# Kernel tuning notes

Hardware: AMD Instinct MI355X
Metric: run time of the kernel (lower is better)

The kernel has to match this reference:

```python
import jax, jax.numpy as jnp
import numpy as np

C_Z = 128
DIST_BINS = 39
MIN_BIN = 3.25
MAX_BIN = 50.75
IN_FEAT = DIST_BINS + 1 + 21 + 21  # 82


def setup_inputs() -> dict:
    key = jax.random.key(0)
    k1, k2, k3, k4, k5 = jax.random.split(key, 5)
    B, T, L = 2, 4, 384
    template_aatype = jax.random.randint(k1, (B, T, L), 0, 21)
    # scale coords so pair distances span the [3.25, 50.75] bin range
    template_ca_coords = 10.0 * jax.random.normal(k2, (B, T, L, 3), dtype=jnp.float32)
    template_ca_mask = jax.random.randint(k3, (B, T, L), 0, 2).astype(bool)
    residue_mask = jnp.ones((B, L), dtype=bool)
    weight = jax.random.normal(k4, (IN_FEAT, C_Z), dtype=jnp.float32) / np.sqrt(IN_FEAT)
    bias = 0.02 * jax.random.normal(k5, (C_Z,), dtype=jnp.float32)
    return dict(template_aatype=template_aatype,
                template_ca_coords=template_ca_coords,
                template_ca_mask=template_ca_mask,
                residue_mask=residue_mask,
                weight=weight, bias=bias)


def reference(template_aatype, template_ca_coords, template_ca_mask, residue_mask, weight, bias):
    # Pairwise CA distances (torch.cdist p=2): [B,T,L,L]
    diff = template_ca_coords[:, :, :, None, :] - template_ca_coords[:, :, None, :, :]
    d = jnp.sqrt(jnp.sum(diff * diff, axis=-1))
    boundaries = jnp.linspace(MIN_BIN, MAX_BIN, DIST_BINS - 1).astype(d.dtype)
    # torch.bucketize(right=False) == searchsorted side='left'
    d_bin = jnp.searchsorted(boundaries, d, side='left')
    aat = jnp.clip(template_aatype, 0, 20)
    # Linear(one_hot concat) == gather of the corresponding weight-row blocks.
    W_d = weight[:DIST_BINS]                       # [39, c_z]
    W_m = weight[DIST_BINS]                        # [c_z]
    W_i = weight[DIST_BINS + 1:DIST_BINS + 22]     # [21, c_z]
    W_j = weight[DIST_BINS + 22:]                  # [21, c_z]
    tmask_pair = (template_ca_mask[:, :, :, None] & template_ca_mask[:, :, None, :]).astype(jnp.float32)  # [B,T,L,L]
    emb = (W_d[d_bin]
           + tmask_pair[..., None] * W_m
           + W_i[aat][:, :, :, None, :]
           + W_j[aat][:, :, None, :, :]
           + bias)                                  # [B,T,L,L,c_z]
    emb = emb * tmask_pair[..., None]
    denom = jnp.maximum(tmask_pair.sum(axis=1), 1.0)[..., None]  # [B,L,L,1]
    z_tpl = emb.sum(axis=1) / denom                 # [B,L,L,c_z]
    res_pair = (residue_mask[:, :, None] & residue_mask[:, None, :]).astype(jnp.float32)[..., None]
    return z_tpl * res_pair
```

## Files before the change

### kernel.cpp

```cpp
#include <hip/hip_runtime.h>
#include <cstddef>

#define BB 2
#define TT 4
#define LL 384
#define CZ 128
#define NBINS 39
#define NBOUND 38

__global__ __launch_bounds__(512) void tpe_kernel(
    const int*   __restrict__ aatype,
    const float* __restrict__ coords,
    const int*   __restrict__ tmask,
    const int*   __restrict__ rmask,
    const float* __restrict__ weight,
    const float* __restrict__ bias,
    float*       __restrict__ out)
{
    __shared__ float Wd_sh[NBINS * CZ];
    __shared__ float Wj_sh[21 * CZ];
    __shared__ float ps_sh[16 * CZ];
    __shared__ int4  meta_sh[LL];

    const int bi  = blockIdx.x;
    const int b   = bi / LL;
    const int i   = bi - b * LL;
    const int tid = threadIdx.x;

    {
        const float4* wsrc = (const float4*)weight;
        float4* wd = (float4*)Wd_sh;
        for (int idx = tid; idx < NBINS * CZ / 4; idx += 512) wd[idx] = wsrc[idx];
        float4* wj = (float4*)Wj_sh;
        for (int idx = tid; idx < 21 * CZ / 4; idx += 512)
            wj[idx] = wsrc[(NBINS + 1 + 21) * CZ / 4 + idx];
    }

    for (int idx = tid; idx < 16 * CZ; idx += 512) {
        int code = idx >> 7, c = idx & (CZ - 1);
        float v = 0.0f;
        if (code) {
            float base = weight[NBINS * CZ + c] + bias[c];
            v = (float)__popc(code) * base;
            #pragma unroll
            for (int t = 0; t < TT; ++t) {
                if (code & (1 << t)) {
                    int aa = aatype[(b * TT + t) * LL + i];
                    aa = min(max(aa, 0), 20);
                    v += weight[(NBINS + 1 + aa) * CZ + c];
                }
            }
        }
        ps_sh[idx] = v;
    }

    {
        #pragma clang fp contract(off)
        const int ri = rmask[b * LL + i];
        for (int j = tid; j < LL; j += 512) {
            unsigned pk01 = 0, pk23 = 0;
            int code = 0;
            #pragma unroll
            for (int t = 0; t < TT; ++t) {
                const int base = (b * TT + t) * LL;
                unsigned pk = 0xFFFFu;
                if (tmask[base + i] != 0 && tmask[base + j] != 0) {
                    const float* ci = coords + (size_t)(base + i) * 3;
                    const float* cj = coords + (size_t)(base + j) * 3;
                    float dx = ci[0] - cj[0];
                    float dy = ci[1] - cj[1];
                    float dz = ci[2] - cj[2];
                    float s  = dx * dx + dy * dy;
                    s = s + dz * dz;
                    float d = sqrtf(s);
                    int bin = 0;
                    #pragma unroll
                    for (int k = 0; k < NBOUND; ++k) {
                        float bnd = (float)(3.25 + (double)k * (47.5 / 37.0));
                        bin += (d > bnd) ? 1 : 0;
                    }
                    int aa = aatype[base + j];
                    aa = min(max(aa, 0), 20);
                    pk = (unsigned)(bin | (aa << 6));
                    code |= (1 << t);
                }
                if (t < 2) pk01 |= pk << (16 * t);
                else       pk23 |= pk << (16 * (t - 2));
            }
            int cnt = __popc(code);
            float scale = (ri != 0 && rmask[b * LL + j] != 0)
                          ? 1.0f / fmaxf((float)cnt, 1.0f) : 0.0f;
            int4 m;
            m.x = (int)pk01; m.y = (int)pk23; m.z = code; m.w = __float_as_int(scale);
            meta_sh[j] = m;
        }
    }
    __syncthreads();

    const int cg = tid & 31;
    const int jj = tid >> 5;
    const float4* Wd4 = (const float4*)Wd_sh;
    const float4* Wj4 = (const float4*)Wj_sh;
    const float4* ps4 = (const float4*)ps_sh;
    float4* outv = (float4*)(out + (size_t)(b * LL + i) * LL * CZ);

    #pragma unroll 2
    for (int j = jj; j < LL; j += 16) {
        int4 m = meta_sh[j];
        const int code = m.z;
        const float scale = __int_as_float(m.w);
        float4 acc = ps4[code * (CZ / 4) + cg];
        const unsigned pk01 = (unsigned)m.x, pk23 = (unsigned)m.y;

        if (code & 1) {
            unsigned pk = pk01 & 0xFFFFu;
            float4 a = Wd4[(pk & 63u) * (CZ / 4) + cg];
            float4 c2 = Wj4[(pk >> 6) * (CZ / 4) + cg];
            acc.x += a.x + c2.x; acc.y += a.y + c2.y; acc.z += a.z + c2.z; acc.w += a.w + c2.w;
        }
        if (code & 2) {
            unsigned pk = pk01 >> 16;
            float4 a = Wd4[(pk & 63u) * (CZ / 4) + cg];
            float4 c2 = Wj4[(pk >> 6) * (CZ / 4) + cg];
            acc.x += a.x + c2.x; acc.y += a.y + c2.y; acc.z += a.z + c2.z; acc.w += a.w + c2.w;
        }
        if (code & 4) {
            unsigned pk = pk23 & 0xFFFFu;
            float4 a = Wd4[(pk & 63u) * (CZ / 4) + cg];
            float4 c2 = Wj4[(pk >> 6) * (CZ / 4) + cg];
            acc.x += a.x + c2.x; acc.y += a.y + c2.y; acc.z += a.z + c2.z; acc.w += a.w + c2.w;
        }
        if (code & 8) {
            unsigned pk = pk23 >> 16;
            float4 a = Wd4[(pk & 63u) * (CZ / 4) + cg];
            float4 c2 = Wj4[(pk >> 6) * (CZ / 4) + cg];
            acc.x += a.x + c2.x; acc.y += a.y + c2.y; acc.z += a.z + c2.z; acc.w += a.w + c2.w;
        }
        float4 o;
        o.x = acc.x * scale; o.y = acc.y * scale;
        o.z = acc.z * scale; o.w = acc.w * scale;
        outv[j * (CZ / 4) + cg] = o;
    }
}

extern "C" void kernel_launch(void* const* d_in, const int* in_sizes, int n_in,
                              void* d_out, int out_size, void* d_ws, size_t ws_size,
                              hipStream_t stream) {
    const int*   aatype = (const int*)d_in[0];
    const float* coords = (const float*)d_in[1];
    const int*   tmask  = (const int*)d_in[2];
    const int*   rmask  = (const int*)d_in[3];
    const float* weight = (const float*)d_in[4];
    const float* bias   = (const float*)d_in[5];
    float* out = (float*)d_out;

    dim3 grid(BB * LL);
    dim3 block(512);
    tpe_kernel<<<grid, block, 0, stream>>>(aatype, coords, tmask, rmask, weight, bias, out);
}
```

Measured before the change: 34.02 us.

## Prefetch weights into registers, compact per-pair template list, nontemporal output stores

Weight rows are loaded into registers at kernel start and written to shared memory only after the metadata pass, so the global-load latency overlaps with the ps table and distance-binning work. Valid templates are packed contiguously with a count, and the four branchy per-template blocks become a counted loop. Output is written with nontemporal stores because it is never reread, and the j loop unroll is raised to 4. In exchange the kernel holds more registers, and the accumulation order of template contributions changes slightly.

```diff
diff --git a/kernel.cpp b/kernel.cpp
--- a/kernel.cpp
+++ b/kernel.cpp
@@ -7,6 +7,8 @@
 #define CZ 128
 #define NBINS 39
 #define NBOUND 38
+
+typedef float f32x4 __attribute__((ext_vector_type(4)));
 
 __global__ __launch_bounds__(512) void tpe_kernel(
     const int*   __restrict__ aatype,
@@ -27,13 +29,13 @@
     const int i   = bi - b * LL;
     const int tid = threadIdx.x;
 
-    {
-        const float4* wsrc = (const float4*)weight;
-        float4* wd = (float4*)Wd_sh;
-        for (int idx = tid; idx < NBINS * CZ / 4; idx += 512) wd[idx] = wsrc[idx];
-        float4* wj = (float4*)Wj_sh;
-        for (int idx = tid; idx < 21 * CZ / 4; idx += 512)
-            wj[idx] = wsrc[(NBINS + 1 + 21) * CZ / 4 + idx];
+    const float4* wsrc = (const float4*)weight;
+    float4 st[4];
+    #pragma unroll
+    for (int k = 0; k < 4; ++k) {
+        int idx = tid + k * 512;
+        if (idx < 1920)
+            st[k] = (idx < 1248) ? wsrc[idx] : wsrc[61 * (CZ / 4) + (idx - 1248)];
     }
 
     for (int idx = tid; idx < 16 * CZ; idx += 512) {
@@ -54,92 +56,84 @@
         ps_sh[idx] = v;
     }
 
+    if (tid < LL) {
+        #pragma clang fp contract(off)
+        const int j  = tid;
+        const int ri = rmask[b * LL + i];
+        unsigned x = 0, y = 0;
+        int code = 0, cnt = 0;
+        #pragma unroll
+        for (int t = 0; t < TT; ++t) {
+            const int base = (b * TT + t) * LL;
+            if (tmask[base + i] != 0 && tmask[base + j] != 0) {
+                const float* ci = coords + (size_t)(base + i) * 3;
+                const float* cj = coords + (size_t)(base + j) * 3;
+                float dx = ci[0] - cj[0];
+                float dy = ci[1] - cj[1];
+                float dz = ci[2] - cj[2];
+                float s  = dx * dx + dy * dy;
+                s = s + dz * dz;
+                float d = sqrtf(s);
+                int bin = 0;
+                #pragma unroll
+                for (int k = 0; k < NBOUND; ++k) {
+                    float bnd = (float)(3.25 + (double)k * (47.5 / 37.0));
+                    bin += (d > bnd) ? 1 : 0;
+                }
+                int aa = aatype[base + j];
+                aa = min(max(aa, 0), 20);
+                unsigned pk = (unsigned)(bin | (aa << 6));
+                if (cnt < 2) x |= pk << (16 * cnt);
+                else         y |= pk << (16 * (cnt - 2));
+                code |= (1 << t);
+                ++cnt;
+            }
+        }
+        float scale = (ri != 0 && rmask[b * LL + j] != 0)
+                      ? 1.0f / fmaxf((float)cnt, 1.0f) : 0.0f;
+        int4 m;
+        m.x = (int)x; m.y = (int)y; m.z = code | (cnt << 8);
+        m.w = __float_as_int(scale);
+        meta_sh[j] = m;
+    }
+
     {
-        #pragma clang fp contract(off)
-        const int ri = rmask[b * LL + i];
-        for (int j = tid; j < LL; j += 512) {
-            unsigned pk01 = 0, pk23 = 0;
-            int code = 0;
-            #pragma unroll
-            for (int t = 0; t < TT; ++t) {
-                const int base = (b * TT + t) * LL;
-                unsigned pk = 0xFFFFu;
-                if (tmask[base + i] != 0 && tmask[base + j] != 0) {
-                    const float* ci = coords + (size_t)(base + i) * 3;
-                    const float* cj = coords + (size_t)(base + j) * 3;
-                    float dx = ci[0] - cj[0];
-                    float dy = ci[1] - cj[1];
-                    float dz = ci[2] - cj[2];
-                    float s  = dx * dx + dy * dy;
-                    s = s + dz * dz;
-                    float d = sqrtf(s);
-                    int bin = 0;
-                    #pragma unroll
-                    for (int k = 0; k < NBOUND; ++k) {
-                        float bnd = (float)(3.25 + (double)k * (47.5 / 37.0));
-                        bin += (d > bnd) ? 1 : 0;
-                    }
-                    int aa = aatype[base + j];
-                    aa = min(max(aa, 0), 20);
-                    pk = (unsigned)(bin | (aa << 6));
-                    code |= (1 << t);
-                }
-                if (t < 2) pk01 |= pk << (16 * t);
-                else       pk23 |= pk << (16 * (t - 2));
+        float4* wd = (float4*)Wd_sh;
+        float4* wj = (float4*)Wj_sh;
+        #pragma unroll
+        for (int k = 0; k < 4; ++k) {
+            int idx = tid + k * 512;
+            if (idx < 1920) {
+                if (idx < 1248) wd[idx] = st[k];
+                else            wj[idx - 1248] = st[k];
             }
-            int cnt = __popc(code);
-            float scale = (ri != 0 && rmask[b * LL + j] != 0)
-                          ? 1.0f / fmaxf((float)cnt, 1.0f) : 0.0f;
-            int4 m;
-            m.x = (int)pk01; m.y = (int)pk23; m.z = code; m.w = __float_as_int(scale);
-            meta_sh[j] = m;
         }
     }
     __syncthreads();
 
     const int cg = tid & 31;
     const int jj = tid >> 5;
-    const float4* Wd4 = (const float4*)Wd_sh;
-    const float4* Wj4 = (const float4*)Wj_sh;
-    const float4* ps4 = (const float4*)ps_sh;
-    float4* outv = (float4*)(out + (size_t)(b * LL + i) * LL * CZ);
+    const f32x4* Wd4 = (const f32x4*)Wd_sh;
+    const f32x4* Wj4 = (const f32x4*)Wj_sh;
+    const f32x4* ps4 = (const f32x4*)ps_sh;
+    f32x4* outv = (f32x4*)(out + (size_t)(b * LL + i) * LL * CZ);
 
-    #pragma unroll 2
+    #pragma unroll 4
     for (int j = jj; j < LL; j += 16) {
         int4 m = meta_sh[j];
-        const int code = m.z;
-        const float scale = __int_as_float(m.w);
-        float4 acc = ps4[code * (CZ / 4) + cg];
-        const unsigned pk01 = (unsigned)m.x, pk23 = (unsigned)m.y;
-
-        if (code & 1) {
-            unsigned pk = pk01 & 0xFFFFu;
-            float4 a = Wd4[(pk & 63u) * (CZ / 4) + cg];
-            float4 c2 = Wj4[(pk >> 6) * (CZ / 4) + cg];
-            acc.x += a.x + c2.x; acc.y += a.y + c2.y; acc.z += a.z + c2.z; acc.w += a.w + c2.w;
+        f32x4 acc = ps4[(m.z & 15) * (CZ / 4) + cg];
+        const int cnt = m.z >> 8;
+        const unsigned x = (unsigned)m.x, y = (unsigned)m.y;
+        for (int k = 0; k < cnt; ++k) {
+            unsigned w2 = (k & 2) ? y : x;
+            unsigned pk = (w2 >> ((k & 1) * 16)) & 0xFFFFu;
+            f32x4 a  = Wd4[(pk & 63u) * (CZ / 4) + cg];
+            f32x4 c2 = Wj4[(pk >> 6) * (CZ / 4) + cg];
+            acc += a + c2;
         }
-        if (code & 2) {
-            unsigned pk = pk01 >> 16;
-            float4 a = Wd4[(pk & 63u) * (CZ / 4) + cg];
-            float4 c2 = Wj4[(pk >> 6) * (CZ / 4) + cg];
-            acc.x += a.x + c2.x; acc.y += a.y + c2.y; acc.z += a.z + c2.z; acc.w += a.w + c2.w;
-        }
-        if (code & 4) {
-            unsigned pk = pk23 & 0xFFFFu;
-            float4 a = Wd4[(pk & 63u) * (CZ / 4) + cg];
-            float4 c2 = Wj4[(pk >> 6) * (CZ / 4) + cg];
-            acc.x += a.x + c2.x; acc.y += a.y + c2.y; acc.z += a.z + c2.z; acc.w += a.w + c2.w;
-        }
-        if (code & 8) {
-            unsigned pk = pk23 >> 16;
-            float4 a = Wd4[(pk & 63u) * (CZ / 4) + cg];
-            float4 c2 = Wj4[(pk >> 6) * (CZ / 4) + cg];
-            acc.x += a.x + c2.x; acc.y += a.y + c2.y; acc.z += a.z + c2.z; acc.w += a.w + c2.w;
-        }
-        float4 o;
-        o.x = acc.x * scale; o.y = acc.y * scale;
-        o.z = acc.z * scale; o.w = acc.w * scale;
-        outv[j * (CZ / 4) + cg] = o;
+        const float s = __int_as_float(m.w);
+        f32x4 o = acc * s;
+        __builtin_nontemporal_store(o, &outv[j * (CZ / 4) + cg]);
     }
 }
 
```

Result: slower. 45.02 us (+32.3%).
